# Kernel tuning notes

Hardware: AMD Instinct MI355X
Metric: run time of the kernel (lower is better)

The kernel has to match this reference:

```python
import jax, jax.numpy as jnp
import numpy as np

FP8_MAX = 448.0
EPS = 1e-12
SCALE_MARGIN = 0.9


def _fp8_quant(t, scale):
    # clamp to e4m3 range, round-trip through float8_e4m3fn to emulate fp8 storage
    q = jnp.clip(t * scale, -FP8_MAX, FP8_MAX)
    return q.astype(jnp.float8_e4m3fn).astype(jnp.float32)


def setup_inputs() -> dict:
    key = jax.random.key(0)
    k1, k2, k3 = jax.random.split(key, 3)
    B, S, K, N = 4, 4096, 2048, 2048
    x = jax.random.normal(k1, (B, S, K), dtype=jnp.float32)
    # kaiming_uniform_(a=sqrt(5)) => U(-1/sqrt(K), 1/sqrt(K)) bound approx; emulate with uniform
    bound_w = 1.0 / np.sqrt(K)
    weight = jax.random.uniform(k2, (N, K), minval=-bound_w, maxval=bound_w, dtype=jnp.float32)
    bound_b = 1.0 / np.sqrt(K)
    bias = jax.random.uniform(k3, (N,), minval=-bound_b, maxval=bound_b, dtype=jnp.float32)
    return {"x": x, "weight": weight, "bias": bias}


def reference(x, weight, bias):
    in_features = weight.shape[1]
    out_features = weight.shape[0]
    # dynamic per-tensor scales (amax history starts at zero -> max == current amax);
    # torch computes these via .item() on buffers => no gradient
    input_scale = jax.lax.stop_gradient(FP8_MAX / (jnp.max(jnp.abs(x)) + EPS) * SCALE_MARGIN)
    weight_scale = jax.lax.stop_gradient(FP8_MAX / (jnp.max(jnp.abs(weight)) + EPS) * SCALE_MARGIN)
    x_fp8 = _fp8_quant(x, input_scale)          # [B, S, K] (fp8-rounded values in fp32)
    w_fp8 = _fp8_quant(weight, weight_scale)    # [N, K]
    out = jnp.matmul(x_fp8.reshape(-1, in_features), w_fp8.T)  # [B*S, N] in fp32
    out = out / (input_scale * weight_scale)
    out = out.reshape(*x.shape[:-1], out_features).astype(x.dtype)
    return out + bias
```

## Files before the change

### kernel.cpp

```cpp
#include <hip/hip_runtime.h>


typedef __attribute__((ext_vector_type(4))) float floatx4;
typedef __attribute__((ext_vector_type(4))) int intx4;
typedef __attribute__((ext_vector_type(8))) int intx8;

#define FP8_MAX_F 448.0f

__device__ __forceinline__ void async_load16(const void* g, void* l) {
    __builtin_amdgcn_global_load_lds(
        (const __attribute__((address_space(1))) unsigned int*)g,
        (__attribute__((address_space(3))) unsigned int*)l,
        16, 0, 0);
}

__device__ __forceinline__ float scale_from_amax(unsigned int bits) {
    return FP8_MAX_F / (__uint_as_float(bits) + 1e-12f) * 0.9f;
}

__global__ __launch_bounds__(256) void amax_both(const float* __restrict__ x,
                                                 long xn4,
                                                 const float* __restrict__ w,
                                                 long wn4, int nbx,
                                                 unsigned int* __restrict__ amax) {
    const float4* src;
    long n4, bid, nblk;
    unsigned int* dst;
    if (blockIdx.x < (unsigned)nbx) {
        src = (const float4*)x; n4 = xn4; dst = amax;     bid = blockIdx.x;       nblk = nbx;
    } else {
        src = (const float4*)w; n4 = wn4; dst = amax + 1; bid = blockIdx.x - nbx; nblk = gridDim.x - nbx;
    }
    long i = bid * blockDim.x + threadIdx.x;
    long stride = nblk * blockDim.x;
    float m = 0.0f;
    for (long j = i; j < n4; j += stride) {
        float4 v = src[j];
        m = fmaxf(m, fmaxf(fmaxf(fabsf(v.x), fabsf(v.y)),
                           fmaxf(fabsf(v.z), fabsf(v.w))));
    }
    #pragma unroll
    for (int off = 32; off > 0; off >>= 1)
        m = fmaxf(m, __shfl_down(m, off));
    __shared__ float wmax[4];
    int lane = threadIdx.x & 63, wid = threadIdx.x >> 6;
    if (lane == 0) wmax[wid] = m;
    __syncthreads();
    if (threadIdx.x == 0) {
        float b = fmaxf(fmaxf(wmax[0], wmax[1]), fmaxf(wmax[2], wmax[3]));
        atomicMax(dst, __float_as_uint(b));
    }
}

__global__ __launch_bounds__(256) void quant_both(const float* __restrict__ x,
                                                  long xn4,
                                                  const float* __restrict__ w,
                                                  long wn4, int nbx,
                                                  const unsigned int* __restrict__ amax,
                                                  unsigned int* __restrict__ xq,
                                                  unsigned int* __restrict__ wq) {
    const float4* src;
    long n4, bid, nblk;
    unsigned int* dst;
    float s;
    if (blockIdx.x < (unsigned)nbx) {
        src = (const float4*)x; n4 = xn4; dst = xq; bid = blockIdx.x;       nblk = nbx;
        s = scale_from_amax(amax[0]);
    } else {
        src = (const float4*)w; n4 = wn4; dst = wq; bid = blockIdx.x - nbx; nblk = gridDim.x - nbx;
        s = scale_from_amax(amax[1]);
    }
    long i = bid * blockDim.x + threadIdx.x;
    long stride = nblk * blockDim.x;
    for (long j = i; j < n4; j += stride) {
        float4 v = src[j];
        float a0 = fminf(fmaxf(v.x * s, -FP8_MAX_F), FP8_MAX_F);
        float a1 = fminf(fmaxf(v.y * s, -FP8_MAX_F), FP8_MAX_F);
        float a2 = fminf(fmaxf(v.z * s, -FP8_MAX_F), FP8_MAX_F);
        float a3 = fminf(fmaxf(v.w * s, -FP8_MAX_F), FP8_MAX_F);
        int p = __builtin_amdgcn_cvt_pk_fp8_f32(a0, a1, 0, false);
        p = __builtin_amdgcn_cvt_pk_fp8_f32(a2, a3, p, true);
        dst[j] = (unsigned int)p;
    }
}

#define BM 128
#define BN 128
#define BKB 128

__global__ __launch_bounds__(256, 3) void gemm_fp8mx(
    const unsigned char* __restrict__ A,
    const unsigned char* __restrict__ B,
    const float* __restrict__ bias,
    const unsigned int* __restrict__ amax,
    float* __restrict__ C,
    int M, int N, int K) {
    __shared__ __align__(16) unsigned char As[BM * BKB];
    __shared__ __align__(16) unsigned char Bs[BN * BKB];

    const int t = threadIdx.x;
    const int lane = t & 63;
    const int w = t >> 6;
    const int bm = blockIdx.y * BM;
    const int bn = blockIdx.x * BN;
    const int wm = (w >> 1) * 64;
    const int wn = (w & 1) * 64;

    floatx4 acc[4][4] = {};

    const int srow = t >> 3;
    const int gcol = ((t & 7) ^ (srow & 7)) * 16;
    const unsigned char* gA = A + (long)(bm + srow) * K + gcol;
    const unsigned char* gB = B + (long)(bn + srow) * K + gcol;
    unsigned char* lA = As + t * 16;
    unsigned char* lB = Bs + t * 16;

    const int fr = lane & 15;
    const int sw = fr & 7;
    const int b0 = (lane >> 4) * 2;
    const int off0 = (b0 ^ sw) * 16;
    const int off1 = ((b0 + 1) ^ sw) * 16;
    const int rowA = (wm + fr) * BKB;
    const int rowB = (wn + fr) * BKB;

    for (int kt = 0; kt < K; kt += BKB) {
        __syncthreads();
        #pragma unroll
        for (int c = 0; c < 4; c++) {
            async_load16(gA + (long)c * 32 * K + kt, lA + c * 4096);
            async_load16(gB + (long)c * 32 * K + kt, lB + c * 4096);
        }
        __syncthreads();

        intx8 bfrag[4];
        #pragma unroll
        for (int j = 0; j < 4; j++) {
            intx4 lo = *(const intx4*)(Bs + rowB + j * 2048 + off0);
            intx4 hi = *(const intx4*)(Bs + rowB + j * 2048 + off1);
            bfrag[j] = (intx8){lo.x, lo.y, lo.z, lo.w, hi.x, hi.y, hi.z, hi.w};
        }
        #pragma unroll
        for (int i = 0; i < 4; i++) {
            intx4 lo = *(const intx4*)(As + rowA + i * 2048 + off0);
            intx4 hi = *(const intx4*)(As + rowA + i * 2048 + off1);
            intx8 afrag = (intx8){lo.x, lo.y, lo.z, lo.w, hi.x, hi.y, hi.z, hi.w};
            #pragma unroll
            for (int j = 0; j < 4; j++)
                acc[i][j] = __builtin_amdgcn_mfma_scale_f32_16x16x128_f8f6f4(
                    afrag, bfrag[j], acc[i][j],
                     0,  0,
                    0, 0x7f7f7f7f, 0, 0x7f7f7f7f);
        }
    }

    const float is = scale_from_amax(amax[0]);
    const float ws = scale_from_amax(amax[1]);
    const float rcp = 1.0f / (is * ws);
    const int crow = bm + wm + (lane >> 4) * 4;
    const int ccol = bn + wn + fr;
    #pragma unroll
    for (int j = 0; j < 4; j++) {
        const int col = ccol + j * 16;
        const float bv = bias[col];
        #pragma unroll
        for (int i = 0; i < 4; i++) {
            const int row0 = crow + i * 16;
            #pragma unroll
            for (int r = 0; r < 4; r++)
                C[(long)(row0 + r) * N + col] = acc[i][j][r] * rcp + bv;
        }
    }
}

extern "C" void kernel_launch(void* const* d_in, const int* in_sizes, int n_in,
                              void* d_out, int out_size, void* d_ws, size_t ws_size,
                              hipStream_t stream) {
    const float* x = (const float*)d_in[0];
    const float* wt = (const float*)d_in[1];
    const float* bias = (const float*)d_in[2];
    float* out = (float*)d_out;

    const int xn = in_sizes[0];
    const int wn = in_sizes[1];
    const int N = in_sizes[2];
    const int K = wn / N;
    const int M = xn / K;

    unsigned char* wsb = (unsigned char*)d_ws;
    unsigned int* amax = (unsigned int*)wsb;
    unsigned char* xq = wsb + 64;
    unsigned char* wq = wsb + 64 + (size_t)xn;

    hipMemsetAsync(amax, 0, 8, stream);
    amax_both<<<2560, 256, 0, stream>>>(x, (long)xn / 4, wt, (long)wn / 4, 2048, amax);
    quant_both<<<2560, 256, 0, stream>>>(x, (long)xn / 4, wt, (long)wn / 4, 2048,
                                         amax, (unsigned int*)xq, (unsigned int*)wq);
    dim3 grid(N / BN, M / BM);
    gemm_fp8mx<<<grid, 256, 0, stream>>>(xq, wq, bias, amax, out, M, N, K);
}
```

Baseline: 367.6 us.

## Fuse amax and quantize into one cooperative kernel; swizzle GEMM blocks; nontemporal stores

Replaces the memset plus separate amax and quantize kernels with one cooperative kernel. It reduces per-block partial maxima, does a grid-wide sync, re-reduces the partials in every block and then quantizes both x and the weight. This removes a launch and the global atomics. The GEMM also remaps block indices in groups of 8 for better L2 locality and writes its output with nontemporal stores. The risks are that the second read of x may miss in cache, and that the partials scratch lives in the output buffer.

```diff
diff --git a/kernel.cpp b/kernel.cpp
--- a/kernel.cpp
+++ b/kernel.cpp
@@ -1,4 +1,7 @@
 #include <hip/hip_runtime.h>
+#include <hip/hip_cooperative_groups.h>
+
+namespace cg = cooperative_groups;
 
 
 typedef __attribute__((ext_vector_type(4))) float floatx4;
@@ -6,6 +9,7 @@
 typedef __attribute__((ext_vector_type(8))) int intx8;
 
 #define FP8_MAX_F 448.0f
+#define SIDE_GRID 1024
 
 __device__ __forceinline__ void async_load16(const void* g, void* l) {
     __builtin_amdgcn_global_load_lds(
@@ -14,73 +18,94 @@
         16, 0, 0);
 }
 
+__device__ __forceinline__ float scale_from_amax_f(float a) {
+    return FP8_MAX_F / (a + 1e-12f) * 0.9f;
+}
 __device__ __forceinline__ float scale_from_amax(unsigned int bits) {
-    return FP8_MAX_F / (__uint_as_float(bits) + 1e-12f) * 0.9f;
-}
-
-__global__ __launch_bounds__(256) void amax_both(const float* __restrict__ x,
-                                                 long xn4,
-                                                 const float* __restrict__ w,
-                                                 long wn4, int nbx,
-                                                 unsigned int* __restrict__ amax) {
-    const float4* src;
-    long n4, bid, nblk;
-    unsigned int* dst;
-    if (blockIdx.x < (unsigned)nbx) {
-        src = (const float4*)x; n4 = xn4; dst = amax;     bid = blockIdx.x;       nblk = nbx;
-    } else {
-        src = (const float4*)w; n4 = wn4; dst = amax + 1; bid = blockIdx.x - nbx; nblk = gridDim.x - nbx;
-    }
-    long i = bid * blockDim.x + threadIdx.x;
-    long stride = nblk * blockDim.x;
-    float m = 0.0f;
-    for (long j = i; j < n4; j += stride) {
-        float4 v = src[j];
-        m = fmaxf(m, fmaxf(fmaxf(fabsf(v.x), fabsf(v.y)),
-                           fmaxf(fabsf(v.z), fabsf(v.w))));
+    return scale_from_amax_f(__uint_as_float(bits));
+}
+
+__global__ __launch_bounds__(256) void amax_quant(
+    const float* __restrict__ x, long xn4,
+    const float* __restrict__ w, long wn4,
+    float* __restrict__ partials,
+    unsigned int* __restrict__ amax,
+    unsigned int* __restrict__ xq,
+    unsigned int* __restrict__ wq) {
+    const float4* xv = (const float4*)x;
+    const float4* wv = (const float4*)w;
+    const long tid = (long)blockIdx.x * 256 + threadIdx.x;
+    const long stride = (long)SIDE_GRID * 256;
+    const int lane = threadIdx.x & 63, wid = threadIdx.x >> 6;
+    __shared__ float red[2][4];
+
+    float mx = 0.0f, mw = 0.0f;
+    for (long j = tid; j < xn4; j += stride) {
+        float4 v = xv[j];
+        mx = fmaxf(mx, fmaxf(fmaxf(fabsf(v.x), fabsf(v.y)),
+                             fmaxf(fabsf(v.z), fabsf(v.w))));
+    }
+    for (long j = tid; j < wn4; j += stride) {
+        float4 v = wv[j];
+        mw = fmaxf(mw, fmaxf(fmaxf(fabsf(v.x), fabsf(v.y)),
+                             fmaxf(fabsf(v.z), fabsf(v.w))));
     }
     #pragma unroll
-    for (int off = 32; off > 0; off >>= 1)
-        m = fmaxf(m, __shfl_down(m, off));
-    __shared__ float wmax[4];
-    int lane = threadIdx.x & 63, wid = threadIdx.x >> 6;
-    if (lane == 0) wmax[wid] = m;
+    for (int off = 32; off > 0; off >>= 1) {
+        mx = fmaxf(mx, __shfl_down(mx, off));
+        mw = fmaxf(mw, __shfl_down(mw, off));
+    }
+    if (lane == 0) { red[0][wid] = mx; red[1][wid] = mw; }
     __syncthreads();
     if (threadIdx.x == 0) {
-        float b = fmaxf(fmaxf(wmax[0], wmax[1]), fmaxf(wmax[2], wmax[3]));
-        atomicMax(dst, __float_as_uint(b));
-    }
-}
-
-__global__ __launch_bounds__(256) void quant_both(const float* __restrict__ x,
-                                                  long xn4,
-                                                  const float* __restrict__ w,
-                                                  long wn4, int nbx,
-                                                  const unsigned int* __restrict__ amax,
-                                                  unsigned int* __restrict__ xq,
-                                                  unsigned int* __restrict__ wq) {
-    const float4* src;
-    long n4, bid, nblk;
-    unsigned int* dst;
-    float s;
-    if (blockIdx.x < (unsigned)nbx) {
-        src = (const float4*)x; n4 = xn4; dst = xq; bid = blockIdx.x;       nblk = nbx;
-        s = scale_from_amax(amax[0]);
-    } else {
-        src = (const float4*)w; n4 = wn4; dst = wq; bid = blockIdx.x - nbx; nblk = gridDim.x - nbx;
-        s = scale_from_amax(amax[1]);
-    }
-    long i = bid * blockDim.x + threadIdx.x;
-    long stride = nblk * blockDim.x;
-    for (long j = i; j < n4; j += stride) {
-        float4 v = src[j];
-        float a0 = fminf(fmaxf(v.x * s, -FP8_MAX_F), FP8_MAX_F);
-        float a1 = fminf(fmaxf(v.y * s, -FP8_MAX_F), FP8_MAX_F);
-        float a2 = fminf(fmaxf(v.z * s, -FP8_MAX_F), FP8_MAX_F);
-        float a3 = fminf(fmaxf(v.w * s, -FP8_MAX_F), FP8_MAX_F);
+        partials[blockIdx.x] =
+            fmaxf(fmaxf(red[0][0], red[0][1]), fmaxf(red[0][2], red[0][3]));
+        partials[SIDE_GRID + blockIdx.x] =
+            fmaxf(fmaxf(red[1][0], red[1][1]), fmaxf(red[1][2], red[1][3]));
+    }
+
+    cg::this_grid().sync();
+
+    mx = 0.0f; mw = 0.0f;
+    for (int p = threadIdx.x; p < SIDE_GRID; p += 256) {
+        mx = fmaxf(mx, partials[p]);
+        mw = fmaxf(mw, partials[SIDE_GRID + p]);
+    }
+    #pragma unroll
+    for (int off = 32; off > 0; off >>= 1) {
+        mx = fmaxf(mx, __shfl_down(mx, off));
+        mw = fmaxf(mw, __shfl_down(mw, off));
+    }
+    if (lane == 0) { red[0][wid] = mx; red[1][wid] = mw; }
+    __syncthreads();
+    mx = fmaxf(fmaxf(red[0][0], red[0][1]), fmaxf(red[0][2], red[0][3]));
+    mw = fmaxf(fmaxf(red[1][0], red[1][1]), fmaxf(red[1][2], red[1][3]));
+    if (blockIdx.x == 0 && threadIdx.x == 0) {
+        amax[0] = __float_as_uint(mx);
+        amax[1] = __float_as_uint(mw);
+    }
+
+    const float sx = scale_from_amax_f(mx);
+    const float sw = scale_from_amax_f(mw);
+    for (long j = tid; j < xn4; j += stride) {
+        float4 v = xv[j];
+        float a0 = fminf(fmaxf(v.x * sx, -FP8_MAX_F), FP8_MAX_F);
+        float a1 = fminf(fmaxf(v.y * sx, -FP8_MAX_F), FP8_MAX_F);
+        float a2 = fminf(fmaxf(v.z * sx, -FP8_MAX_F), FP8_MAX_F);
+        float a3 = fminf(fmaxf(v.w * sx, -FP8_MAX_F), FP8_MAX_F);
         int p = __builtin_amdgcn_cvt_pk_fp8_f32(a0, a1, 0, false);
         p = __builtin_amdgcn_cvt_pk_fp8_f32(a2, a3, p, true);
-        dst[j] = (unsigned int)p;
+        xq[j] = (unsigned int)p;
+    }
+    for (long j = tid; j < wn4; j += stride) {
+        float4 v = wv[j];
+        float a0 = fminf(fmaxf(v.x * sw, -FP8_MAX_F), FP8_MAX_F);
+        float a1 = fminf(fmaxf(v.y * sw, -FP8_MAX_F), FP8_MAX_F);
+        float a2 = fminf(fmaxf(v.z * sw, -FP8_MAX_F), FP8_MAX_F);
+        float a3 = fminf(fmaxf(v.w * sw, -FP8_MAX_F), FP8_MAX_F);
+        int p = __builtin_amdgcn_cvt_pk_fp8_f32(a0, a1, 0, false);
+        p = __builtin_amdgcn_cvt_pk_fp8_f32(a2, a3, p, true);
+        wq[j] = (unsigned int)p;
     }
 }
 
@@ -101,8 +126,13 @@
     const int t = threadIdx.x;
     const int lane = t & 63;
     const int w = t >> 6;
-    const int bm = blockIdx.y * BM;
-    const int bn = blockIdx.x * BN;
+
+    int flat = blockIdx.y * gridDim.x + blockIdx.x;
+    const int nwg = gridDim.x * gridDim.y;
+    if ((nwg & 7) == 0) flat = (flat & 7) * (nwg >> 3) + (flat >> 3);
+    const int bm = (flat / gridDim.x) * BM;
+    const int bn = (flat % gridDim.x) * BN;
+
     const int wm = (w >> 1) * 64;
     const int wn = (w & 1) * 64;
 
@@ -167,7 +197,8 @@
             const int row0 = crow + i * 16;
             #pragma unroll
             for (int r = 0; r < 4; r++)
-                C[(long)(row0 + r) * N + col] = acc[i][j][r] * rcp + bv;
+                __builtin_nontemporal_store(acc[i][j][r] * rcp + bv,
+                                            &C[(long)(row0 + r) * N + col]);
         }
     }
 }
@@ -191,10 +222,17 @@
     unsigned char* xq = wsb + 64;
     unsigned char* wq = wsb + 64 + (size_t)xn;
 
-    hipMemsetAsync(amax, 0, 8, stream);
-    amax_both<<<2560, 256, 0, stream>>>(x, (long)xn / 4, wt, (long)wn / 4, 2048, amax);
-    quant_both<<<2560, 256, 0, stream>>>(x, (long)xn / 4, wt, (long)wn / 4, 2048,
-                                         amax, (unsigned int*)xq, (unsigned int*)wq);
+    float* partials = out;
+    long xn4 = (long)xn / 4, wn4 = (long)wn / 4;
+    const float* xa = x;
+    const float* wa = wt;
+    unsigned int* xqa = (unsigned int*)xq;
+    unsigned int* wqa = (unsigned int*)wq;
+    void* kargs[] = {(void*)&xa, (void*)&xn4, (void*)&wa, (void*)&wn4,
+                     (void*)&partials, (void*)&amax, (void*)&xqa, (void*)&wqa};
+    hipLaunchCooperativeKernel((void*)amax_quant, dim3(SIDE_GRID), dim3(256),
+                               kargs, 0, stream);
+
     dim3 grid(N / BN, M / BM);
     gemm_fp8mx<<<grid, 256, 0, stream>>>(xq, wq, bias, amax, out, M, N, K);
 }
```

Result: slower. 430.0 us (+17.0%).
